# Kernel tuning notes

Hardware: AMD Instinct MI355X
Metric: run time of the kernel (lower is better)

Reference implementation:

```python
import jax, jax.numpy as jnp
import numpy as np

B, T, H = 2, 4096, 2048
NH, HD, INTER, K = 16, 128, 8192, 3
BASE = 10000.0
EPS = 1e-6


def setup_inputs() -> dict:
    key = jax.random.key(0)
    ks = jax.random.split(key, 10)
    s = 0.02
    return {
        "hidden_states": jax.random.normal(ks[0], (B, T, H), jnp.float32),
        "position_ids": jnp.tile(jnp.arange(T, dtype=jnp.int32)[None, :], (B, 1)),
        "conv_w": jax.random.normal(ks[1], (H, H, K), jnp.float32) * s,  # OIH
        "conv_b": jnp.zeros((H,), jnp.float32),
        "wq": jax.random.normal(ks[2], (H, NH * HD), jnp.float32) * s,
        "wv": jax.random.normal(ks[3], (H, NH * HD), jnp.float32) * s,
        "w_dt": jax.random.normal(ks[4], (H, NH), jnp.float32) * s,
        "b_dt": jnp.zeros((NH,), jnp.float32),
        "A_log": jnp.full((NH,), -4.0, jnp.float32),
        "dt_bias": jnp.full((NH,), -2.0, jnp.float32),
        "wo": jax.random.normal(ks[5], (NH * HD, H), jnp.float32) * s,
        "w1": jax.random.normal(ks[6], (H, INTER), jnp.float32) * s,
        "w2": jax.random.normal(ks[7], (INTER, H), jnp.float32) * s,
        "norm1_w": jnp.ones((H,), jnp.float32),
        "norm2_w": jnp.ones((H,), jnp.float32),
    }


def _rmsnorm(x, w):
    return x * jax.lax.rsqrt(jnp.mean(x * x, axis=-1, keepdims=True) + EPS) * w


def _causal_conv(x, conv_w, conv_b):
    # x: [B,T,H] -> NCH conv with left pad (causal)
    xc = jnp.transpose(x, (0, 2, 1))  # [B,H,T]
    y = jax.lax.conv_general_dilated(
        xc, conv_w, window_strides=(1,), padding=[(K - 1, 0)],
        dimension_numbers=("NCH", "OIH", "NCH"))
    y = y + conv_b[None, :, None]
    return jnp.transpose(y, (0, 2, 1))  # [B,T,H]


def _rope(q, position_ids):
    # q: [B,NH,T,HD]; matches the torch interleaved-rotate + concatenated cos/sin
    inv_freq = 1.0 / (BASE ** (jnp.arange(0, HD, 2, dtype=jnp.float32) / HD))
    freqs = position_ids.astype(jnp.float32)[..., None] * inv_freq  # [B,T,HD/2]
    emb = jnp.concatenate([freqs, freqs], axis=-1)                   # [B,T,HD]
    cos = jnp.cos(emb)[:, None]  # [B,1,T,HD]
    sin = jnp.sin(emb)[:, None]
    x1, x2 = q[..., ::2], q[..., 1::2]
    x_rot = jnp.stack([-x2, x1], axis=-1).reshape(q.shape)
    return q * cos + x_rot * sin


def _gated_deltanet(h, position_ids, conv_w, conv_b, wq, wv, w_dt, b_dt, A_log, dt_bias, wo):
    x = _causal_conv(h, conv_w, conv_b)  # [B,T,H]
    q = (x @ wq).reshape(B, T, NH, HD).transpose(0, 2, 1, 3)  # [B,NH,T,HD]
    v = (x @ wv).reshape(B, T, NH, HD).transpose(0, 2, 1, 3)
    q = _rope(q, position_ids)
    dt_raw = (h @ w_dt + b_dt).transpose(0, 2, 1)  # [B,NH,T]
    dt = jax.nn.softplus(dt_raw + dt_bias[None, :, None])
    A = -jnp.exp(A_log)[None, :, None]
    alpha = jnp.exp(A * dt)
    beta = dt
    p = jnp.cumprod(alpha, axis=2)                 # [B,NH,T]
    u = beta[..., None] * v / (p[..., None] + EPS)  # [B,NH,T,HD]
    s = jnp.cumsum(u, axis=2)
    state = p[..., None] * s
    out = (q * state).transpose(0, 2, 1, 3).reshape(B, T, NH * HD)
    return out @ wo


def reference(hidden_states, position_ids, conv_w, conv_b, wq, wv, w_dt, b_dt,
              A_log, dt_bias, wo, w1, w2, norm1_w, norm2_w):
    # pre-norm residual decoder layer: attn block then MLP block
    attn_in = _rmsnorm(hidden_states, norm1_w)
    h = hidden_states + _gated_deltanet(attn_in, position_ids, conv_w, conv_b,
                                        wq, wv, w_dt, b_dt, A_log, dt_bias, wo)
    mlp_in = _rmsnorm(h, norm2_w)
    out = h + (jax.nn.silu(mlp_in @ w1) @ w2)
    return out
```

## Files before the change

kernel.cpp:

```cpp
#include <hip/hip_runtime.h>
#include <stdint.h>

#define T_DIM 4096
#define H_DIM 2048
#define NHEADS 16
#define HD_DIM 128
#define INTER_DIM 8192
#define B_DIM 2
#define MROWS (B_DIM * T_DIM)
#define NCHUNK 32
#define CHUNK (T_DIM / NCHUNK)

typedef unsigned short ushort_t;
typedef _Float16 f16x8 __attribute__((ext_vector_type(8)));
typedef __attribute__((ext_vector_type(4))) float f32x4;

__device__ __forceinline__ ushort_t f2h(float f) {
    union { _Float16 h; ushort_t u; } x;
    x.h = (_Float16)f;
    return x.u;
}
__device__ __forceinline__ float h2f(ushort_t u) {
    union { ushort_t u; _Float16 h; } x;
    x.u = u;
    return (float)x.h;
}

__device__ __forceinline__ void stage16(const ushort_t* g, ushort_t* lbase) {
#if __has_builtin(__builtin_amdgcn_global_load_lds)
    __builtin_amdgcn_global_load_lds(
        (__attribute__((address_space(1))) unsigned int*)g,
        (__attribute__((address_space(3))) unsigned int*)lbase,
        16, 0, 0);
#else
    ((f16x8*)lbase)[threadIdx.x & 63] = *(const f16x8*)g;
#endif
}

template <int EPI, int SHIFTS>
__global__ __launch_bounds__(256) void gemm_f16(
    const ushort_t* __restrict__ A,
    const ushort_t* __restrict__ B0,
    const ushort_t* __restrict__ B1,
    const ushort_t* __restrict__ B2,
    const float* __restrict__ bias,
    const float* addsrc,
    float* outf,
    ushort_t* outb,
    int M, int N, int K, int lda, int ldb)
{
    __shared__ __align__(16) ushort_t Asm[128 * 64];
    __shared__ __align__(16) ushort_t Bsm[128 * 64];

    const int tid  = threadIdx.x;
    const int lane = tid & 63;
    const int wave = tid >> 6;
    const int m0 = blockIdx.y * 128;
    const int n0 = blockIdx.x * 128;
    const int wm = (wave >> 1) * 64;
    const int wn = (wave & 1) * 64;
    const int m16 = lane & 15;
    const int q4  = lane >> 4;
    const int l7  = lane & 7;
    const int srow = lane >> 3;
    const int soct = (lane & 7) ^ srow;

    f32x4 acc[4][4];
#pragma unroll
    for (int i = 0; i < 4; i++)
#pragma unroll
        for (int j = 0; j < 4; j++)
#pragma unroll
            for (int r = 0; r < 4; r++) acc[i][j][r] = 0.f;

    for (int s = 0; s < SHIFTS; s++) {
        const ushort_t* Abase;
        if (SHIFTS == 3) {
            int b = m0 >> 12;
            Abase = A + (size_t)(m0 + 2 * b + s) * lda;
        } else {
            Abase = A + (size_t)m0 * lda;
        }
        const ushort_t* Bs = (s == 0) ? B0 : ((s == 1) ? B1 : B2);
        const ushort_t* Bbase = Bs + (size_t)n0 * ldb;

        for (int k0 = 0; k0 < K; k0 += 64) {
            __syncthreads();
#pragma unroll
            for (int c = 0; c < 4; c++) {
                int ck = wave * 4 + c;
                const ushort_t* ga = Abase + (size_t)(ck * 8 + srow) * lda + (k0 + soct * 8);
                stage16(ga, &Asm[ck * 512]);
                const ushort_t* gb = Bbase + (size_t)(ck * 8 + srow) * ldb + (k0 + soct * 8);
                stage16(gb, &Bsm[ck * 512]);
            }
            __syncthreads();
#pragma unroll
            for (int kk = 0; kk < 2; kk++) {
                f16x8 af[4], bfv[4];
                int oc = kk * 4 + q4;
#pragma unroll
                for (int mi = 0; mi < 4; mi++) {
                    int row = wm + mi * 16 + m16;
                    af[mi] = *(const f16x8*)&Asm[row * 64 + ((oc ^ l7) << 3)];
                }
#pragma unroll
                for (int ni = 0; ni < 4; ni++) {
                    int row = wn + ni * 16 + m16;
                    bfv[ni] = *(const f16x8*)&Bsm[row * 64 + ((oc ^ l7) << 3)];
                }
#pragma unroll
                for (int mi = 0; mi < 4; mi++)
#pragma unroll
                    for (int ni = 0; ni < 4; ni++)
                        acc[mi][ni] = __builtin_amdgcn_mfma_f32_16x16x32_f16(
                            af[mi], bfv[ni], acc[mi][ni], 0, 0, 0);
            }
        }
    }

#pragma unroll
    for (int mi = 0; mi < 4; mi++) {
#pragma unroll
        for (int ni = 0; ni < 4; ni++) {
            int col = n0 + wn + ni * 16 + m16;
#pragma unroll
            for (int r = 0; r < 4; r++) {
                int row = m0 + wm + mi * 16 + q4 * 4 + r;
                size_t idx = (size_t)row * N + col;
                float v = acc[mi][ni][r];
                if (EPI == 1) {
                    outf[idx] = v;
                } else if (EPI == 2) {
                    outb[idx] = f2h(v + bias[col]);
                } else if (EPI == 3) {
                    outf[idx] = addsrc[idx] + v;
                } else if (EPI == 4) {
                    outb[idx] = f2h(v / (1.f + expf(-v)));
                } else if (EPI == 5) {
                    outb[idx] = f2h(v);
                }
            }
        }
    }
}

__global__ void transpose_to_f16(const float* __restrict__ in, ushort_t* __restrict__ out,
                                 int R, int C) {
    __shared__ float tile[32][33];
    int c0 = blockIdx.x * 32, r0 = blockIdx.y * 32;
    int tx = threadIdx.x, ty = threadIdx.y;
#pragma unroll
    for (int j = 0; j < 32; j += 8)
        tile[ty + j][tx] = in[(size_t)(r0 + ty + j) * C + c0 + tx];
    __syncthreads();
#pragma unroll
    for (int j = 0; j < 32; j += 8)
        out[(size_t)(c0 + ty + j) * R + r0 + tx] = f2h(tile[tx][ty + j]);
}

__global__ void conv_w_convert(const float* __restrict__ cw, ushort_t* __restrict__ w0,
                               ushort_t* __restrict__ w1, ushort_t* __restrict__ w2) {
    int gid = blockIdx.x * 256 + threadIdx.x;
    const float* p = cw + (size_t)gid * 3;
    w0[gid] = f2h(p[0]);
    w1[gid] = f2h(p[1]);
    w2[gid] = f2h(p[2]);
}

__global__ __launch_bounds__(256) void rmsnorm_kernel(const float* __restrict__ x,
                                                      const float* __restrict__ w,
                                                      ushort_t* __restrict__ out, int pad) {
    int r = blockIdx.x;
    int tid = threadIdx.x;
    const float* row = x + (size_t)r * H_DIM;
    float xs[8];
    *(float4*)&xs[0] = *(const float4*)&row[tid * 8];
    *(float4*)&xs[4] = *(const float4*)&row[tid * 8 + 4];
    float ss = 0.f;
#pragma unroll
    for (int e = 0; e < 8; e++) ss += xs[e] * xs[e];
#pragma unroll
    for (int o = 32; o >= 1; o >>= 1) ss += __shfl_down(ss, o, 64);
    __shared__ float red[4];
    if ((tid & 63) == 0) red[tid >> 6] = ss;
    __syncthreads();
    float rs = rsqrtf((red[0] + red[1] + red[2] + red[3]) * (1.f / 2048.f) + 1e-6f);
    float ws[8];
    *(float4*)&ws[0] = *(const float4*)&w[tid * 8];
    *(float4*)&ws[4] = *(const float4*)&w[tid * 8 + 4];
    ushort_t* orow;
    if (pad) {
        int b = r >> 12, t = r & 4095;
        orow = out + ((size_t)b * (T_DIM + 2) + 2 + t) * H_DIM;
        if (t == 0) {
            ushort_t* pz = out + (size_t)b * (T_DIM + 2) * H_DIM;
            for (int e = tid; e < 2 * H_DIM; e += 256) pz[e] = 0;
        }
    } else {
        orow = out + (size_t)r * H_DIM;
    }
#pragma unroll
    for (int e = 0; e < 8; e++) orow[tid * 8 + e] = f2h(xs[e] * rs * ws[e]);
}

__global__ __launch_bounds__(256) void dt_kernel(const ushort_t* __restrict__ apad,
                                                 const float* __restrict__ wdt,
                                                 const float* __restrict__ bdt,
                                                 const float* __restrict__ dtb,
                                                 float* __restrict__ beta_arr) {
    int r = blockIdx.x;
    int b = r >> 12, t = r & 4095;
    int tid = threadIdx.x, lane = tid & 63, wv = tid >> 6;
    const ushort_t* row = apad + ((size_t)b * (T_DIM + 2) + 2 + t) * H_DIM;
    float acc[16];
#pragma unroll
    for (int nh = 0; nh < 16; nh++) acc[nh] = 0.f;
    f16x8 xv = *(const f16x8*)&row[tid * 8];
#pragma unroll
    for (int e = 0; e < 8; e++) {
        float x = (float)xv[e];
        const float* wrow = wdt + (size_t)(tid * 8 + e) * 16;
#pragma unroll
        for (int nh = 0; nh < 16; nh++) acc[nh] += x * wrow[nh];
    }
    __shared__ float part[4][16];
#pragma unroll
    for (int nh = 0; nh < 16; nh++) {
        float v = acc[nh];
#pragma unroll
        for (int o = 32; o >= 1; o >>= 1) v += __shfl_down(v, o, 64);
        if (lane == 0) part[wv][nh] = v;
    }
    __syncthreads();
    if (tid < 16) {
        float v = part[0][tid] + part[1][tid] + part[2][tid] + part[3][tid];
        float x = v + bdt[tid] + dtb[tid];
        float dt = (x > 20.f) ? x : log1pf(expf(x));
        beta_arr[(size_t)(b * 16 + tid) * T_DIM + t] = dt;
    }
}

__global__ __launch_bounds__(256) void scan_prep(const float* __restrict__ beta_arr,
                                                 const float* __restrict__ A_log,
                                                 float* __restrict__ p_arr,
                                                 float* __restrict__ c_arr) {
    int bh = blockIdx.x;
    int nh = bh & 15;
    int tid = threadIdx.x;
    float Ac = -expf(A_log[nh]);
    size_t base = (size_t)bh * T_DIM;
    float bet[16], pref[16];
    float run = 0.f;
#pragma unroll
    for (int j = 0; j < 16; j++) {
        bet[j] = beta_arr[base + tid * 16 + j];
        run += Ac * bet[j];
        pref[j] = run;
    }
    __shared__ float red[256];
    red[tid] = run;
    __syncthreads();
    if (tid == 0) {
        float a = 0.f;
        for (int i = 0; i < 256; i++) { float x = red[i]; red[i] = a; a += x; }
    }
    __syncthreads();
    float off = red[tid];
#pragma unroll
    for (int j = 0; j < 16; j++) {
        float p = expf(off + pref[j]);
        p_arr[base + tid * 16 + j] = p;
        c_arr[base + tid * 16 + j] = bet[j] / (p + 1e-6f);
    }
}

__global__ __launch_bounds__(128) void scan_partial(const float* __restrict__ c_arr,
                                                    const ushort_t* __restrict__ v_buf,
                                                    float* __restrict__ csum) {
    int blk = blockIdx.x;
    int ch = blk & (NCHUNK - 1), bh = blk >> 5;
    int b = bh >> 4, nh = bh & 15;
    int tid = threadIdx.x;
    int t0 = ch * CHUNK;
    __shared__ float cs[CHUNK];
    cs[tid] = c_arr[(size_t)bh * T_DIM + t0 + tid];
    __syncthreads();
    float s = 0.f;
    const ushort_t* vbase = v_buf + ((size_t)(b * T_DIM + t0) * 16 + nh) * 128 + tid;
    for (int tt = 0; tt < CHUNK; tt++) s += cs[tt] * h2f(vbase[(size_t)tt * 2048]);
    csum[(size_t)blk * 128 + tid] = s;
}

__global__ __launch_bounds__(128) void scan_combine(const float* __restrict__ csum,
                                                    float* __restrict__ cpref) {
    int bh = blockIdx.x;
    int tid = threadIdx.x;
    float run = 0.f;
    for (int ch = 0; ch < NCHUNK; ch++) {
        size_t i = ((size_t)bh * NCHUNK + ch) * 128 + tid;
        cpref[i] = run;
        run += csum[i];
    }
}

__global__ __launch_bounds__(128) void scan_final(const float* __restrict__ c_arr,
                                                  const float* __restrict__ p_arr,
                                                  const ushort_t* __restrict__ v_buf,
                                                  const ushort_t* __restrict__ q_buf,
                                                  const float* __restrict__ cpref,
                                                  ushort_t* __restrict__ y_head) {
    int blk = blockIdx.x;
    int ch = blk & (NCHUNK - 1), bh = blk >> 5;
    int b = bh >> 4, nh = bh & 15;
    int tid = threadIdx.x;
    int t0 = ch * CHUNK;
    __shared__ float cs[CHUNK], ps[CHUNK];
    cs[tid] = c_arr[(size_t)bh * T_DIM + t0 + tid];
    ps[tid] = p_arr[(size_t)bh * T_DIM + t0 + tid];
    __syncthreads();
    float s = cpref[(size_t)blk * 128 + tid];
    size_t vb = ((size_t)(b * T_DIM + t0) * 16 + nh) * 128 + tid;
    for (int tt = 0; tt < CHUNK; tt++) {
        size_t vi = vb + (size_t)tt * 2048;
        s += cs[tt] * h2f(v_buf[vi]);
        float y = h2f(q_buf[vi]) * (ps[tt] * s);
        y_head[vi] = f2h(y);
    }
}

__global__ __launch_bounds__(256) void rope_f16(ushort_t* __restrict__ q,
                                                const int* __restrict__ pos_ids) {
    int gid = blockIdx.x * 256 + threadIdx.x;
    int j = gid & 63;
    int rest = gid >> 6;
    int bt = rest >> 4;
    size_t idx = (size_t)bt * 2048 + (size_t)(rest & 15) * 128 + 2 * j;
    float pos = (float)pos_ids[bt];
    const float LN = 0.14391157f;
    int d0 = 2 * j, d1 = 2 * j + 1;
    float a0 = pos * expf(-(float)(d0 & 63) * LN);
    float a1 = pos * expf(-(float)(d1 & 63) * LN);
    float q0 = h2f(q[idx]), q1 = h2f(q[idx + 1]);
    q[idx]     = f2h(q0 * cosf(a0) - q1 * sinf(a0));
    q[idx + 1] = f2h(q1 * cosf(a1) + q0 * sinf(a1));
}

extern "C" void kernel_launch(void* const* d_in, const int* in_sizes, int n_in,
                              void* d_out, int out_size, void* d_ws, size_t ws_size,
                              hipStream_t stream) {
    (void)in_sizes; (void)n_in; (void)out_size;
    const float* hidden  = (const float*)d_in[0];
    const int*   pos_ids = (const int*)d_in[1];
    const float* conv_w  = (const float*)d_in[2];
    const float* conv_b  = (const float*)d_in[3];
    const float* wq      = (const float*)d_in[4];
    const float* wv      = (const float*)d_in[5];
    const float* w_dt    = (const float*)d_in[6];
    const float* b_dt    = (const float*)d_in[7];
    const float* A_log   = (const float*)d_in[8];
    const float* dt_bias = (const float*)d_in[9];
    const float* wo      = (const float*)d_in[10];
    const float* w1      = (const float*)d_in[11];
    const float* w2      = (const float*)d_in[12];
    const float* n1w     = (const float*)d_in[13];
    const float* n2w     = (const float*)d_in[14];
    float* out = (float*)d_out;

    constexpr size_t MB8 = 8ull * 1024 * 1024;
    constexpr size_t SCAN_SM = 524288;
    constexpr size_t R0   = 0;
    constexpr size_t R0sz = 10 * MB8;
    constexpr size_t R1   = R0 + R0sz;
    constexpr size_t R1sz = 8 * MB8;
    constexpr size_t R2   = R1 + R1sz;
    constexpr size_t R2sz = (size_t)B_DIM * (T_DIM + 2) * H_DIM * 2;
    constexpr size_t R3   = R2 + R2sz;
    constexpr size_t R3sz = 4 * MB8;
    constexpr size_t R4   = R3 + R3sz;
    constexpr size_t R4sz = 4 * MB8;
    constexpr size_t R5   = R4 + R4sz;
    constexpr size_t R5sz = 5 * SCAN_SM;
    constexpr size_t NEED = R5 + R5sz;
    if (ws_size < NEED) return;

    char* w = (char*)d_ws;
    ushort_t* wc0    = (ushort_t*)(w + R0 + 0 * MB8);
    ushort_t* wc1    = (ushort_t*)(w + R0 + 1 * MB8);
    ushort_t* wc2    = (ushort_t*)(w + R0 + 2 * MB8);
    ushort_t* wq_t   = (ushort_t*)(w + R0 + 3 * MB8);
    ushort_t* wv_t   = (ushort_t*)(w + R0 + 4 * MB8);
    ushort_t* wo_t   = (ushort_t*)(w + R0 + 5 * MB8);
    ushort_t* xb     = (ushort_t*)(w + R0 + 6 * MB8);
    ushort_t* a_half = (ushort_t*)(w + R0);
    ushort_t* qb     = (ushort_t*)(w + R1);
    ushort_t* vb     = (ushort_t*)(w + R1 + 4 * MB8);
    float*    h_buf  = (float*)(w + R1);
    ushort_t* apad   = (ushort_t*)(w + R2);
    ushort_t* w1_t   = (ushort_t*)(w + R3);
    ushort_t* w2_t   = (ushort_t*)(w + R4);
    float*    beta   = (float*)(w + R5 + 0 * SCAN_SM);
    float*    parr   = (float*)(w + R5 + 1 * SCAN_SM);
    float*    carr   = (float*)(w + R5 + 2 * SCAN_SM);
    float*    csum   = (float*)(w + R5 + 3 * SCAN_SM);
    float*    cprf   = (float*)(w + R5 + 4 * SCAN_SM);
    ushort_t* mlp_in = apad;
    ushort_t* y_head = xb;

    conv_w_convert<<<(2048 * 2048) / 256, 256, 0, stream>>>(conv_w, wc0, wc1, wc2);
    transpose_to_f16<<<dim3(64, 64), dim3(32, 8), 0, stream>>>(wq, wq_t, 2048, 2048);
    transpose_to_f16<<<dim3(64, 64), dim3(32, 8), 0, stream>>>(wv, wv_t, 2048, 2048);
    transpose_to_f16<<<dim3(64, 64), dim3(32, 8), 0, stream>>>(wo, wo_t, 2048, 2048);
    transpose_to_f16<<<dim3(256, 64), dim3(32, 8), 0, stream>>>(w1, w1_t, 2048, 8192);
    transpose_to_f16<<<dim3(64, 256), dim3(32, 8), 0, stream>>>(w2, w2_t, 8192, 2048);

    rmsnorm_kernel<<<MROWS, 256, 0, stream>>>(hidden, n1w, apad, 1);
    dt_kernel<<<MROWS, 256, 0, stream>>>(apad, w_dt, b_dt, dt_bias, beta);
    scan_prep<<<B_DIM * NHEADS, 256, 0, stream>>>(beta, A_log, parr, carr);

    gemm_f16<2, 3><<<dim3(16, 64), 256, 0, stream>>>(
        apad, wc0, wc1, wc2, conv_b, nullptr, nullptr, xb,
        MROWS, 2048, 2048, 2048, 2048);
    gemm_f16<5, 1><<<dim3(16, 64), 256, 0, stream>>>(
        xb, wq_t, wq_t, wq_t, nullptr, nullptr, nullptr, qb,
        MROWS, 2048, 2048, 2048, 2048);
    gemm_f16<5, 1><<<dim3(16, 64), 256, 0, stream>>>(
        xb, wv_t, wv_t, wv_t, nullptr, nullptr, nullptr, vb,
        MROWS, 2048, 2048, 2048, 2048);
    rope_f16<<<(MROWS * NHEADS * 64) / 256, 256, 0, stream>>>(qb, pos_ids);

    scan_partial<<<B_DIM * NHEADS * NCHUNK, 128, 0, stream>>>(carr, vb, csum);
    scan_combine<<<B_DIM * NHEADS, 128, 0, stream>>>(csum, cprf);
    scan_final<<<B_DIM * NHEADS * NCHUNK, 128, 0, stream>>>(carr, parr, vb, qb, cprf, y_head);

    gemm_f16<3, 1><<<dim3(16, 64), 256, 0, stream>>>(
        y_head, wo_t, wo_t, wo_t, nullptr, hidden, h_buf, nullptr,
        MROWS, 2048, 2048, 2048, 2048);
    rmsnorm_kernel<<<MROWS, 256, 0, stream>>>(h_buf, n2w, mlp_in, 0);

    for (int ha = 0; ha < 2; ha++) {
        gemm_f16<4, 1><<<dim3(32, 64), 256, 0, stream>>>(
            mlp_in, w1_t + (size_t)ha * 4096 * 2048, nullptr, nullptr,
            nullptr, nullptr, nullptr, a_half,
            MROWS, 4096, 2048, 2048, 2048);
        gemm_f16<3, 1><<<dim3(16, 64), 256, 0, stream>>>(
            a_half, w2_t + (size_t)ha * 4096, nullptr, nullptr,
            nullptr, (ha == 0) ? h_buf : out, out, nullptr,
            MROWS, 2048, 4096, 4096, 8192);
    }
}
```

Before: 1.881 ms.

## Replace 128x128 GEMM with double-buffered 256x256 pipelined kernel

Replaces the 128x128-tile, 4-wave GEMM with a 256x256-tile, 8-wave kernel. It double-buffers LDS and splits each k-step's global-to-LDS staging into four groups, interleaved with quadrant MFMA blocks under partial vmcnt barriers. It also adds an XCD-aware block-index swizzle and raises MFMA issue priority with s_setprio. The aim is to hide load latency and raise arithmetic intensity per byte staged. In exchange it uses 128KB of LDS and many more accumulator registers, and it relies on power-of-two grid dimensions for the swizzle.

```diff
diff --git a/kernel.cpp b/kernel.cpp
--- a/kernel.cpp
+++ b/kernel.cpp
@@ -37,8 +37,96 @@
 #endif
 }
 
+__device__ __forceinline__ void vm4_barrier() {
+    asm volatile("s_waitcnt vmcnt(4)\n\ts_barrier" ::: "memory");
+}
+__device__ __forceinline__ void vm0_barrier() {
+    asm volatile("s_waitcnt vmcnt(0)\n\ts_barrier" ::: "memory");
+}
+
+
+template <int G, int SHIFTS>
+__device__ __forceinline__ void stage_group(
+    int t,
+    const ushort_t* __restrict__ A,
+    const ushort_t* __restrict__ B0, const ushort_t* __restrict__ B1,
+    const ushort_t* __restrict__ B2,
+    ushort_t* AsmW, ushort_t* BsmW,
+    int m0, int n0, int lda, int ldb, int KT, int wave, int srow, int soct)
+{
+    int s, kt;
+    if (SHIFTS == 3) {
+        s = (t >= 2 * KT) ? 2 : (t >= KT ? 1 : 0);
+        kt = t - s * KT;
+    } else { s = 0; kt = t; }
+    const int k0 = kt << 6;
+    const ushort_t* Abase;
+    if (SHIFTS == 3) {
+        int b = m0 >> 12;
+        Abase = A + (size_t)(m0 + 2 * b + s) * lda + k0;
+    } else {
+        Abase = A + (size_t)m0 * lda + k0;
+    }
+    const ushort_t* Bp = (SHIFTS == 3) ? ((s == 0) ? B0 : ((s == 1) ? B1 : B2)) : B0;
+    const ushort_t* Bbase = Bp + (size_t)n0 * ldb + k0;
+#pragma unroll
+    for (int l = 0; l < 2; ++l) {
+        const int j = wave * 2 + l;
+        int chunk;
+        const ushort_t* base;
+        int ld;
+        ushort_t* dst;
+        if (G == 0) {
+            if (j < 8) { chunk = j; base = Abase; ld = lda; dst = AsmW; }
+            else { int jj = j - 8; chunk = (jj & 3) + ((jj >> 2) << 3); base = Bbase; ld = ldb; dst = BsmW; }
+        } else if (G == 1) {
+            if (j < 8) { chunk = 16 + j; base = Abase; ld = lda; dst = AsmW; }
+            else { int jj = j - 8; chunk = 16 + (jj & 3) + ((jj >> 2) << 3); base = Bbase; ld = ldb; dst = BsmW; }
+        } else if (G == 2) {
+            chunk = 4 + (j & 3) + ((j >> 2) << 3); base = Bbase; ld = ldb; dst = BsmW;
+        } else {
+            chunk = 8 + (j & 7) + ((j >> 3) << 4); base = Abase; ld = lda; dst = AsmW;
+        }
+        stage16(base + (size_t)(chunk * 8 + srow) * ld + soct * 8, dst + chunk * 512);
+    }
+}
+
+#define LOAD_A(MH)                                                             \
+    _Pragma("unroll")                                                          \
+    for (int mi = 0; mi < 4; ++mi)                                             \
+    _Pragma("unroll")                                                          \
+    for (int kk = 0; kk < 2; ++kk) {                                           \
+        const int row_ = wm + (MH) * 64 + mi * 16 + m16;                       \
+        af[mi * 2 + kk] =                                                      \
+            *(const f16x8*)&Ar[row_ * 64 + (((kk * 4 + q4) ^ l7) << 3)];       \
+    }
+
+#define LOAD_B(NH)                                                             \
+    _Pragma("unroll")                                                          \
+    for (int ni = 0; ni < 2; ++ni)                                             \
+    _Pragma("unroll")                                                          \
+    for (int kk = 0; kk < 2; ++kk) {                                           \
+        const int row_ = wn + (NH) * 32 + ni * 16 + m16;                       \
+        bfv[((NH) * 2 + ni) * 2 + kk] =                                        \
+            *(const f16x8*)&Br[row_ * 64 + (((kk * 4 + q4) ^ l7) << 3)];       \
+    }
+
+#define MFMA_Q(MH, NH)                                                         \
+    __builtin_amdgcn_s_setprio(1);                                             \
+    _Pragma("unroll")                                                          \
+    for (int mi = 0; mi < 4; ++mi)                                             \
+    _Pragma("unroll")                                                          \
+    for (int ni = 0; ni < 2; ++ni)                                             \
+    _Pragma("unroll")                                                          \
+    for (int kk = 0; kk < 2; ++kk)                                             \
+        acc[(MH) * 4 + mi][(NH) * 2 + ni] =                                    \
+            __builtin_amdgcn_mfma_f32_16x16x32_f16(                            \
+                af[mi * 2 + kk], bfv[((NH) * 2 + ni) * 2 + kk],                \
+                acc[(MH) * 4 + mi][(NH) * 2 + ni], 0, 0, 0);                   \
+    __builtin_amdgcn_s_setprio(0);
+
 template <int EPI, int SHIFTS>
-__global__ __launch_bounds__(256) void gemm_f16(
+__global__ __launch_bounds__(512, 2) void gemm256(
     const ushort_t* __restrict__ A,
     const ushort_t* __restrict__ B0,
     const ushort_t* __restrict__ B1,
@@ -49,86 +137,101 @@
     ushort_t* outb,
     int M, int N, int K, int lda, int ldb)
 {
-    __shared__ __align__(16) ushort_t Asm[128 * 64];
-    __shared__ __align__(16) ushort_t Bsm[128 * 64];
+    __shared__ __align__(16) ushort_t Abuf[2 * 16384];
+    __shared__ __align__(16) ushort_t Bbuf[2 * 16384];
 
     const int tid  = threadIdx.x;
     const int lane = tid & 63;
     const int wave = tid >> 6;
-    const int m0 = blockIdx.y * 128;
-    const int n0 = blockIdx.x * 128;
-    const int wm = (wave >> 1) * 64;
-    const int wn = (wave & 1) * 64;
+
+    const int nwg = gridDim.x * gridDim.y;
+    const int bid = blockIdx.y * gridDim.x + blockIdx.x;
+    const int swz = (bid & 7) * (nwg >> 3) + (bid >> 3);
+    const int gxl = 31 - __clz((int)gridDim.x);
+    const int bx  = swz & ((int)gridDim.x - 1);
+    const int by  = swz >> gxl;
+
+    const int m0 = by * 256;
+    const int n0 = bx * 256;
+    const int wm = (wave >> 2) * 128;
+    const int wn = (wave & 3) * 64;
     const int m16 = lane & 15;
     const int q4  = lane >> 4;
     const int l7  = lane & 7;
     const int srow = lane >> 3;
     const int soct = (lane & 7) ^ srow;
 
-    f32x4 acc[4][4];
-#pragma unroll
-    for (int i = 0; i < 4; i++)
+    const int KT = K >> 6;
+    const int NT = SHIFTS * KT;
+
+    f32x4 acc[8][4];
+#pragma unroll
+    for (int i = 0; i < 8; i++)
 #pragma unroll
         for (int j = 0; j < 4; j++)
 #pragma unroll
             for (int r = 0; r < 4; r++) acc[i][j][r] = 0.f;
 
-    for (int s = 0; s < SHIFTS; s++) {
-        const ushort_t* Abase;
-        if (SHIFTS == 3) {
-            int b = m0 >> 12;
-            Abase = A + (size_t)(m0 + 2 * b + s) * lda;
-        } else {
-            Abase = A + (size_t)m0 * lda;
-        }
-        const ushort_t* Bs = (s == 0) ? B0 : ((s == 1) ? B1 : B2);
-        const ushort_t* Bbase = Bs + (size_t)n0 * ldb;
-
-        for (int k0 = 0; k0 < K; k0 += 64) {
-            __syncthreads();
-#pragma unroll
-            for (int c = 0; c < 4; c++) {
-                int ck = wave * 4 + c;
-                const ushort_t* ga = Abase + (size_t)(ck * 8 + srow) * lda + (k0 + soct * 8);
-                stage16(ga, &Asm[ck * 512]);
-                const ushort_t* gb = Bbase + (size_t)(ck * 8 + srow) * ldb + (k0 + soct * 8);
-                stage16(gb, &Bsm[ck * 512]);
-            }
-            __syncthreads();
-#pragma unroll
-            for (int kk = 0; kk < 2; kk++) {
-                f16x8 af[4], bfv[4];
-                int oc = kk * 4 + q4;
-#pragma unroll
-                for (int mi = 0; mi < 4; mi++) {
-                    int row = wm + mi * 16 + m16;
-                    af[mi] = *(const f16x8*)&Asm[row * 64 + ((oc ^ l7) << 3)];
-                }
-#pragma unroll
-                for (int ni = 0; ni < 4; ni++) {
-                    int row = wn + ni * 16 + m16;
-                    bfv[ni] = *(const f16x8*)&Bsm[row * 64 + ((oc ^ l7) << 3)];
-                }
-#pragma unroll
-                for (int mi = 0; mi < 4; mi++)
-#pragma unroll
-                    for (int ni = 0; ni < 4; ni++)
-                        acc[mi][ni] = __builtin_amdgcn_mfma_f32_16x16x32_f16(
-                            af[mi], bfv[ni], acc[mi][ni], 0, 0, 0);
-            }
-        }
-    }
-
-#pragma unroll
-    for (int mi = 0; mi < 4; mi++) {
-#pragma unroll
-        for (int ni = 0; ni < 4; ni++) {
-            int col = n0 + wn + ni * 16 + m16;
-#pragma unroll
-            for (int r = 0; r < 4; r++) {
-                int row = m0 + wm + mi * 16 + q4 * 4 + r;
-                size_t idx = (size_t)row * N + col;
-                float v = acc[mi][ni][r];
+    f16x8 af[8];
+    f16x8 bfv[8];
+
+    stage_group<0, SHIFTS>(0, A, B0, B1, B2, Abuf, Bbuf, m0, n0, lda, ldb, KT, wave, srow, soct);
+    stage_group<1, SHIFTS>(0, A, B0, B1, B2, Abuf, Bbuf, m0, n0, lda, ldb, KT, wave, srow, soct);
+    stage_group<2, SHIFTS>(0, A, B0, B1, B2, Abuf, Bbuf, m0, n0, lda, ldb, KT, wave, srow, soct);
+    stage_group<3, SHIFTS>(0, A, B0, B1, B2, Abuf, Bbuf, m0, n0, lda, ldb, KT, wave, srow, soct);
+    vm4_barrier();
+
+    for (int t = 0; t < NT - 1; ++t) {
+        const ushort_t* Ar = Abuf + (t & 1) * 16384;
+        const ushort_t* Br = Bbuf + (t & 1) * 16384;
+        ushort_t* Aw = Abuf + ((t + 1) & 1) * 16384;
+        ushort_t* Bw = Bbuf + ((t + 1) & 1) * 16384;
+
+        stage_group<0, SHIFTS>(t + 1, A, B0, B1, B2, Aw, Bw, m0, n0, lda, ldb, KT, wave, srow, soct);
+        LOAD_A(0)
+        LOAD_B(0)
+        MFMA_Q(0, 0)
+        vm4_barrier();
+
+        stage_group<1, SHIFTS>(t + 1, A, B0, B1, B2, Aw, Bw, m0, n0, lda, ldb, KT, wave, srow, soct);
+        LOAD_B(1)
+        MFMA_Q(0, 1)
+        vm4_barrier();
+
+        stage_group<2, SHIFTS>(t + 1, A, B0, B1, B2, Aw, Bw, m0, n0, lda, ldb, KT, wave, srow, soct);
+        LOAD_A(1)
+        MFMA_Q(1, 0)
+        vm4_barrier();
+
+        stage_group<3, SHIFTS>(t + 1, A, B0, B1, B2, Aw, Bw, m0, n0, lda, ldb, KT, wave, srow, soct);
+        MFMA_Q(1, 1)
+        vm4_barrier();
+    }
+
+    vm0_barrier();
+    {
+        const ushort_t* Ar = Abuf + ((NT - 1) & 1) * 16384;
+        const ushort_t* Br = Bbuf + ((NT - 1) & 1) * 16384;
+        LOAD_A(0)
+        LOAD_B(0)
+        MFMA_Q(0, 0)
+        LOAD_B(1)
+        MFMA_Q(0, 1)
+        LOAD_A(1)
+        MFMA_Q(1, 0)
+        MFMA_Q(1, 1)
+    }
+
+#pragma unroll
+    for (int a = 0; a < 8; ++a) {
+#pragma unroll
+        for (int b = 0; b < 4; ++b) {
+            const int col = n0 + wn + b * 16 + m16;
+#pragma unroll
+            for (int r = 0; r < 4; ++r) {
+                const int row = m0 + wm + a * 16 + q4 * 4 + r;
+                const size_t idx = (size_t)row * N + col;
+                float v = acc[a][b][r];
                 if (EPI == 1) {
                     outf[idx] = v;
                 } else if (EPI == 2) {
@@ -144,6 +247,10 @@
         }
     }
 }
+
+#undef LOAD_A
+#undef LOAD_B
+#undef MFMA_Q
 
 __global__ void transpose_to_f16(const float* __restrict__ in, ushort_t* __restrict__ out,
                                  int R, int C) {
@@ -418,13 +525,13 @@
     dt_kernel<<<MROWS, 256, 0, stream>>>(apad, w_dt, b_dt, dt_bias, beta);
     scan_prep<<<B_DIM * NHEADS, 256, 0, stream>>>(beta, A_log, parr, carr);
 
-    gemm_f16<2, 3><<<dim3(16, 64), 256, 0, stream>>>(
+    gemm256<2, 3><<<dim3(8, 32), 512, 0, stream>>>(
         apad, wc0, wc1, wc2, conv_b, nullptr, nullptr, xb,
         MROWS, 2048, 2048, 2048, 2048);
-    gemm_f16<5, 1><<<dim3(16, 64), 256, 0, stream>>>(
+    gemm256<5, 1><<<dim3(8, 32), 512, 0, stream>>>(
         xb, wq_t, wq_t, wq_t, nullptr, nullptr, nullptr, qb,
         MROWS, 2048, 2048, 2048, 2048);
-    gemm_f16<5, 1><<<dim3(16, 64), 256, 0, stream>>>(
+    gemm256<5, 1><<<dim3(8, 32), 512, 0, stream>>>(
         xb, wv_t, wv_t, wv_t, nullptr, nullptr, nullptr, vb,
         MROWS, 2048, 2048, 2048, 2048);
     rope_f16<<<(MROWS * NHEADS * 64) / 256, 256, 0, stream>>>(qb, pos_ids);
@@ -433,17 +540,17 @@
     scan_combine<<<B_DIM * NHEADS, 128, 0, stream>>>(csum, cprf);
     scan_final<<<B_DIM * NHEADS * NCHUNK, 128, 0, stream>>>(carr, parr, vb, qb, cprf, y_head);
 
-    gemm_f16<3, 1><<<dim3(16, 64), 256, 0, stream>>>(
+    gemm256<3, 1><<<dim3(8, 32), 512, 0, stream>>>(
         y_head, wo_t, wo_t, wo_t, nullptr, hidden, h_buf, nullptr,
         MROWS, 2048, 2048, 2048, 2048);
     rmsnorm_kernel<<<MROWS, 256, 0, stream>>>(h_buf, n2w, mlp_in, 0);
 
     for (int ha = 0; ha < 2; ha++) {
-        gemm_f16<4, 1><<<dim3(32, 64), 256, 0, stream>>>(
+        gemm256<4, 1><<<dim3(16, 32), 512, 0, stream>>>(
             mlp_in, w1_t + (size_t)ha * 4096 * 2048, nullptr, nullptr,
             nullptr, nullptr, nullptr, a_half,
             MROWS, 4096, 2048, 2048, 2048);
-        gemm_f16<3, 1><<<dim3(16, 64), 256, 0, stream>>>(
+        gemm256<3, 1><<<dim3(8, 32), 512, 0, stream>>>(
             a_half, w2_t + (size_t)ha * 4096, nullptr, nullptr,
             nullptr, (ha == 0) ? h_buf : out, out, nullptr,
             MROWS, 2048, 4096, 4096, 8192);
```

New measurement: 1.867 ms. About the same (-0.7%).

## Replace 128x128 GEMM with double-buffered 256x256 tile GEMM and block swizzle

Applied to the files above, without the earlier changes.

Swaps the single-buffered 128x128 f16 MFMA GEMM for a 512-thread 256x256 tile kernel. It double-buffers LDS, interleaves async global-to-LDS staging with MFMA phases using partial vmcnt barriers and s_setprio, and remaps block IDs in a swizzled order for better cache locality. The aim is to hide global load latency and raise arithmetic intensity per tile. In exchange it uses more LDS and more registers, needs a grid dimension that is a power of two, and relies on hand-tuned waitcnt counts that must match the exact number of loads issued.

```diff
diff --git a/kernel.cpp b/kernel.cpp
--- a/kernel.cpp
+++ b/kernel.cpp
@@ -37,8 +37,104 @@
 #endif
 }
 
+__device__ __forceinline__ void vm4_barrier() {
+    asm volatile("s_waitcnt vmcnt(4)\n\ts_barrier" ::: "memory");
+}
+__device__ __forceinline__ void vm2_barrier() {
+    asm volatile("s_waitcnt vmcnt(2)\n\ts_barrier" ::: "memory");
+}
+__device__ __forceinline__ void vm0_barrier() {
+    asm volatile("s_waitcnt vmcnt(0)\n\ts_barrier" ::: "memory");
+}
+
+
+#define PH_STAGE_A0(W)                                                        \
+    if (STG) {                                                                \
+        stage16(gAs,          &Asm[(W) * 16384 + wave * 1024]);               \
+        stage16(gAs + lda8,   &Asm[(W) * 16384 + wave * 1024 + 512]);         \
+    }
+#define PH_STAGE_B0(W)                                                        \
+    if (STG) {                                                                \
+        stage16(gBs,          &Bsm[(W) * 16384 + wave * 1024]);               \
+        stage16(gBs + ldb8,   &Bsm[(W) * 16384 + wave * 1024 + 512]);         \
+    }
+#define PH_STAGE_B1(W)                                                        \
+    if (STG) {                                                                \
+        stage16(gBs + ldb128, &Bsm[(W) * 16384 + 8192 + wave * 1024]);        \
+        stage16(gBs + ldb136, &Bsm[(W) * 16384 + 8192 + wave * 1024 + 512]);  \
+    }
+#define PH_STAGE_A1(W)                                                        \
+    if (STG) {                                                                \
+        stage16(gAs + lda128, &Asm[(W) * 16384 + 8192 + wave * 1024]);        \
+        stage16(gAs + lda136, &Asm[(W) * 16384 + 8192 + wave * 1024 + 512]);  \
+    }
+
+#define LDS_A(R, HA)                                                          \
+    _Pragma("unroll")                                                         \
+    for (int mi = 0; mi < 4; ++mi) {                                          \
+        af[mi * 2 + 0] = *(const f16x8*)&Asm[(R) * 16384 + (HA) * 8192 +      \
+                                             mi * 1024 + rdA0];               \
+        af[mi * 2 + 1] = *(const f16x8*)&Asm[(R) * 16384 + (HA) * 8192 +      \
+                                             mi * 1024 + rdA1];               \
+    }
+#define LDS_B(R, HB)                                                          \
+    _Pragma("unroll")                                                         \
+    for (int ni = 0; ni < 2; ++ni) {                                          \
+        bf[ni * 2 + 0] = *(const f16x8*)&Bsm[(R) * 16384 + (HB) * 8192 +      \
+                                             ni * 1024 + rdB0];               \
+        bf[ni * 2 + 1] = *(const f16x8*)&Bsm[(R) * 16384 + (HB) * 8192 +      \
+                                             ni * 1024 + rdB1];               \
+    }
+#define MF(HA, HB)                                                            \
+    __builtin_amdgcn_s_setprio(1);                                            \
+    _Pragma("unroll")                                                         \
+    for (int mi = 0; mi < 4; ++mi)                                            \
+    _Pragma("unroll")                                                         \
+    for (int ni = 0; ni < 2; ++ni)                                            \
+    _Pragma("unroll")                                                         \
+    for (int kk = 0; kk < 2; ++kk)                                            \
+        acc[(HA) * 4 + mi][(HB) * 2 + ni] =                                   \
+            __builtin_amdgcn_mfma_f32_16x16x32_f16(                           \
+                af[mi * 2 + kk], bf[ni * 2 + kk],                             \
+                acc[(HA) * 4 + mi][(HB) * 2 + ni], 0, 0, 0);                  \
+    __builtin_amdgcn_s_setprio(0);
+
+#define ADVANCE()                                                             \
+    {                                                                         \
+        gAs += 64;                                                            \
+        ++ts;                                                                 \
+        if (SHIFTS == 3 && (ts & (KT - 1)) == 0 && ts < NT) {                 \
+            gBs = (ts == KT) ? gBp1 : gBp2;                                   \
+        } else {                                                              \
+            gBs += 64;                                                        \
+        }                                                                     \
+    }
+
+#define TILE(R, STG)                                                          \
+    {                                                                         \
+        PH_STAGE_A0(1 - (R))                                                  \
+        LDS_A(R, 0)                                                           \
+        LDS_B(R, 0)                                                           \
+        MF(0, 0)                                                              \
+        if (STG) vm4_barrier(); else vm2_barrier();                           \
+        PH_STAGE_B0(1 - (R))                                                  \
+        LDS_B(R, 1)                                                           \
+        MF(0, 1)                                                              \
+        if (STG) vm4_barrier(); else vm0_barrier();                           \
+        PH_STAGE_B1(1 - (R))                                                  \
+        LDS_A(R, 1)                                                           \
+        MF(1, 1)                                                              \
+        PH_STAGE_A1(1 - (R))                                                  \
+        LDS_B(R, 0)                                                           \
+        MF(1, 0)                                                              \
+        if (STG) {                                                            \
+            vm4_barrier();                                                    \
+            ADVANCE()                                                         \
+        }                                                                     \
+    }
+
 template <int EPI, int SHIFTS>
-__global__ __launch_bounds__(256) void gemm_f16(
+__global__ __launch_bounds__(512, 2) void gemm256(
     const ushort_t* __restrict__ A,
     const ushort_t* __restrict__ B0,
     const ushort_t* __restrict__ B1,
@@ -49,86 +145,94 @@
     ushort_t* outb,
     int M, int N, int K, int lda, int ldb)
 {
-    __shared__ __align__(16) ushort_t Asm[128 * 64];
-    __shared__ __align__(16) ushort_t Bsm[128 * 64];
+    __shared__ __align__(16) ushort_t Asm[2 * 16384];
+    __shared__ __align__(16) ushort_t Bsm[2 * 16384];
 
     const int tid  = threadIdx.x;
     const int lane = tid & 63;
     const int wave = tid >> 6;
-    const int m0 = blockIdx.y * 128;
-    const int n0 = blockIdx.x * 128;
-    const int wm = (wave >> 1) * 64;
-    const int wn = (wave & 1) * 64;
+
+    const int nwg = gridDim.x * gridDim.y;
+    const int bid = blockIdx.y * gridDim.x + blockIdx.x;
+    const int swz = (bid & 7) * (nwg >> 3) + (bid >> 3);
+    const int gxl = 31 - __clz((int)gridDim.x);
+    const int bx  = swz & ((int)gridDim.x - 1);
+    const int by  = swz >> gxl;
+
+    const int m0 = by * 256;
+    const int n0 = bx * 256;
+    const int wm2 = (wave >> 2) * 64;
+    const int wn2 = (wave & 3) * 32;
     const int m16 = lane & 15;
     const int q4  = lane >> 4;
     const int l7  = lane & 7;
     const int srow = lane >> 3;
     const int soct = (lane & 7) ^ srow;
 
-    f32x4 acc[4][4];
-#pragma unroll
-    for (int i = 0; i < 4; i++)
+    const int KT = K >> 6;
+    const int NT = SHIFTS * KT;
+
+    const int rdA0 = (wm2 + m16) * 64 + (q4 ^ l7) * 8;
+    const int rdA1 = rdA0 ^ 32;
+    const int rdB0 = (wn2 + m16) * 64 + (q4 ^ l7) * 8;
+    const int rdB1 = rdB0 ^ 32;
+
+    const size_t lda8 = (size_t)lda * 8,  lda128 = (size_t)lda * 128, lda136 = (size_t)lda * 136;
+    const size_t ldb8 = (size_t)ldb * 8,  ldb128 = (size_t)ldb * 128, ldb136 = (size_t)ldb * 136;
+    const size_t athr = (size_t)(wave * 16 + srow) * lda + soct * 8;
+    const size_t bthr = (size_t)(wave * 16 + srow) * ldb + soct * 8;
+    const ushort_t* gAs;
+    if (SHIFTS == 3) {
+        int b = m0 >> 12;
+        gAs = A + (size_t)(m0 + 2 * b) * lda + athr;
+    } else {
+        gAs = A + (size_t)m0 * lda + athr;
+    }
+    const ushort_t* gBs  = B0 + (size_t)n0 * ldb + bthr;
+    const ushort_t* gBp1 = (SHIFTS == 3) ? (B1 + (size_t)n0 * ldb + bthr) : nullptr;
+    const ushort_t* gBp2 = (SHIFTS == 3) ? (B2 + (size_t)n0 * ldb + bthr) : nullptr;
+    int ts = 0;
+
+    f32x4 acc[8][4];
+#pragma unroll
+    for (int i = 0; i < 8; i++)
 #pragma unroll
         for (int j = 0; j < 4; j++)
 #pragma unroll
             for (int r = 0; r < 4; r++) acc[i][j][r] = 0.f;
 
-    for (int s = 0; s < SHIFTS; s++) {
-        const ushort_t* Abase;
-        if (SHIFTS == 3) {
-            int b = m0 >> 12;
-            Abase = A + (size_t)(m0 + 2 * b + s) * lda;
-        } else {
-            Abase = A + (size_t)m0 * lda;
-        }
-        const ushort_t* Bs = (s == 0) ? B0 : ((s == 1) ? B1 : B2);
-        const ushort_t* Bbase = Bs + (size_t)n0 * ldb;
-
-        for (int k0 = 0; k0 < K; k0 += 64) {
-            __syncthreads();
-#pragma unroll
-            for (int c = 0; c < 4; c++) {
-                int ck = wave * 4 + c;
-                const ushort_t* ga = Abase + (size_t)(ck * 8 + srow) * lda + (k0 + soct * 8);
-                stage16(ga, &Asm[ck * 512]);
-                const ushort_t* gb = Bbase + (size_t)(ck * 8 + srow) * ldb + (k0 + soct * 8);
-                stage16(gb, &Bsm[ck * 512]);
-            }
-            __syncthreads();
-#pragma unroll
-            for (int kk = 0; kk < 2; kk++) {
-                f16x8 af[4], bfv[4];
-                int oc = kk * 4 + q4;
-#pragma unroll
-                for (int mi = 0; mi < 4; mi++) {
-                    int row = wm + mi * 16 + m16;
-                    af[mi] = *(const f16x8*)&Asm[row * 64 + ((oc ^ l7) << 3)];
-                }
-#pragma unroll
-                for (int ni = 0; ni < 4; ni++) {
-                    int row = wn + ni * 16 + m16;
-                    bfv[ni] = *(const f16x8*)&Bsm[row * 64 + ((oc ^ l7) << 3)];
-                }
-#pragma unroll
-                for (int mi = 0; mi < 4; mi++)
-#pragma unroll
-                    for (int ni = 0; ni < 4; ni++)
-                        acc[mi][ni] = __builtin_amdgcn_mfma_f32_16x16x32_f16(
-                            af[mi], bfv[ni], acc[mi][ni], 0, 0, 0);
-            }
-        }
-    }
-
-#pragma unroll
-    for (int mi = 0; mi < 4; mi++) {
-#pragma unroll
-        for (int ni = 0; ni < 4; ni++) {
-            int col = n0 + wn + ni * 16 + m16;
-#pragma unroll
-            for (int r = 0; r < 4; r++) {
-                int row = m0 + wm + mi * 16 + q4 * 4 + r;
-                size_t idx = (size_t)row * N + col;
-                float v = acc[mi][ni][r];
+    f16x8 af[8];
+    f16x8 bf[4];
+
+    {
+        const bool STG = true;
+        PH_STAGE_A0(0)
+        PH_STAGE_B0(0)
+        PH_STAGE_B1(0)
+        PH_STAGE_A1(0)
+        ADVANCE()
+    }
+    vm4_barrier();
+
+    for (int t = 0; t < NT - 2; t += 2) {
+        { const bool STG = true; TILE(0, STG) }
+        { const bool STG = true; TILE(1, STG) }
+    }
+    { const bool STG = true;  TILE(0, STG) }
+    { const bool STG = false; TILE(1, STG) }
+
+#pragma unroll
+    for (int a = 0; a < 8; ++a) {
+        const int ha = a >> 2, mi = a & 3;
+#pragma unroll
+        for (int b = 0; b < 4; ++b) {
+            const int hb = b >> 1, ni = b & 1;
+            const int col = n0 + hb * 128 + wn2 + ni * 16 + m16;
+#pragma unroll
+            for (int r = 0; r < 4; ++r) {
+                const int row = m0 + ha * 128 + wm2 + mi * 16 + q4 * 4 + r;
+                const size_t idx = (size_t)row * N + col;
+                float v = acc[a][b][r];
                 if (EPI == 1) {
                     outf[idx] = v;
                 } else if (EPI == 2) {
@@ -144,6 +248,16 @@
         }
     }
 }
+
+#undef PH_STAGE_A0
+#undef PH_STAGE_B0
+#undef PH_STAGE_B1
+#undef PH_STAGE_A1
+#undef LDS_A
+#undef LDS_B
+#undef MF
+#undef ADVANCE
+#undef TILE
 
 __global__ void transpose_to_f16(const float* __restrict__ in, ushort_t* __restrict__ out,
                                  int R, int C) {
@@ -418,13 +532,13 @@
     dt_kernel<<<MROWS, 256, 0, stream>>>(apad, w_dt, b_dt, dt_bias, beta);
     scan_prep<<<B_DIM * NHEADS, 256, 0, stream>>>(beta, A_log, parr, carr);
 
-    gemm_f16<2, 3><<<dim3(16, 64), 256, 0, stream>>>(
+    gemm256<2, 3><<<dim3(8, 32), 512, 0, stream>>>(
         apad, wc0, wc1, wc2, conv_b, nullptr, nullptr, xb,
         MROWS, 2048, 2048, 2048, 2048);
-    gemm_f16<5, 1><<<dim3(16, 64), 256, 0, stream>>>(
+    gemm256<5, 1><<<dim3(8, 32), 512, 0, stream>>>(
         xb, wq_t, wq_t, wq_t, nullptr, nullptr, nullptr, qb,
         MROWS, 2048, 2048, 2048, 2048);
-    gemm_f16<5, 1><<<dim3(16, 64), 256, 0, stream>>>(
+    gemm256<5, 1><<<dim3(8, 32), 512, 0, stream>>>(
         xb, wv_t, wv_t, wv_t, nullptr, nullptr, nullptr, vb,
         MROWS, 2048, 2048, 2048, 2048);
     rope_f16<<<(MROWS * NHEADS * 64) / 256, 256, 0, stream>>>(qb, pos_ids);
@@ -433,17 +547,17 @@
     scan_combine<<<B_DIM * NHEADS, 128, 0, stream>>>(csum, cprf);
     scan_final<<<B_DIM * NHEADS * NCHUNK, 128, 0, stream>>>(carr, parr, vb, qb, cprf, y_head);
 
-    gemm_f16<3, 1><<<dim3(16, 64), 256, 0, stream>>>(
+    gemm256<3, 1><<<dim3(8, 32), 512, 0, stream>>>(
         y_head, wo_t, wo_t, wo_t, nullptr, hidden, h_buf, nullptr,
         MROWS, 2048, 2048, 2048, 2048);
     rmsnorm_kernel<<<MROWS, 256, 0, stream>>>(h_buf, n2w, mlp_in, 0);
 
     for (int ha = 0; ha < 2; ha++) {
-        gemm_f16<4, 1><<<dim3(32, 64), 256, 0, stream>>>(
+        gemm256<4, 1><<<dim3(16, 32), 512, 0, stream>>>(
             mlp_in, w1_t + (size_t)ha * 4096 * 2048, nullptr, nullptr,
             nullptr, nullptr, nullptr, a_half,
             MROWS, 4096, 2048, 2048, 2048);
-        gemm_f16<3, 1><<<dim3(16, 64), 256, 0, stream>>>(
+        gemm256<3, 1><<<dim3(8, 32), 512, 0, stream>>>(
             a_half, w2_t + (size_t)ha * 4096, nullptr, nullptr,
             nullptr, (ha == 0) ? h_buf : out, out, nullptr,
             MROWS, 2048, 4096, 4096, 8192);
```

Result: faster. 1.653 ms (-12.1%).
